# Optimization experiments

Hardware: AMD Instinct MI355X
Metric: run time of the kernel (lower is better)

The kernel has to match this reference:

```python
import jax, jax.numpy as jnp
import numpy as np

N = 2048   # nodes
E = 65536  # edges (avg degree 32)
F = 7      # node_feature_dim
S = 32     # state_dim
L = 16     # latent_dim
R = 3      # message passing rounds


def setup_inputs() -> dict:
    key = jax.random.key(0)
    ks = jax.random.split(key, 12)
    g = lambda k, shape, s: (jax.random.normal(k, shape, jnp.float32) * s)
    return dict(
        x=g(ks[0], (N, F), 1.0),
        edge_index=jax.random.randint(ks[1], (2, E), 0, N, dtype=jnp.int32),
        # input_net Linear(F->S)
        W_in=g(ks[2], (F, S), 0.3), b_in=jnp.zeros((S,), jnp.float32),
        # message nets: R x Linear(S->S)
        W_msg=g(ks[3], (R, S, S), 0.15), b_msg=jnp.zeros((R, S), jnp.float32),
        # GRU cells: R x (weight_ih, weight_hh) stored (in, 3*S) with torch gate order r,z,n
        W_ih=g(ks[4], (R, S, 3 * S), 0.15), W_hh=g(ks[5], (R, S, 3 * S), 0.15),
        b_ih=jnp.zeros((R, 3 * S), jnp.float32), b_hh=jnp.zeros((R, 3 * S), jnp.float32),
        # mu / logstd heads Linear(S->L)
        W_mu=g(ks[6], (S, L), 0.15), b_mu=jnp.zeros((L,), jnp.float32),
        W_ls=g(ks[7], (S, L), 0.15), b_ls=jnp.zeros((L,), jnp.float32),
        # decoder: Linear(2L->L), ReLU, Linear(L->1)
        W_d1=g(ks[8], (2 * L, L), 0.2), b_d1=jnp.zeros((L,), jnp.float32),
        W_d2=g(ks[9], (L, 1), 0.2), b_d2=jnp.zeros((1,), jnp.float32),
    )


def reference(x, edge_index, W_in, b_in, W_msg, b_msg, W_ih, W_hh, b_ih, b_hh,
              W_mu, b_mu, W_ls, b_ls, W_d1, b_d1, W_d2, b_d2):
    src, dst = edge_index[0], edge_index[1]
    # encoder
    state = jax.nn.relu(x @ W_in + b_in)  # [N, S]
    for r in range(R):
        message = jax.nn.relu(state @ W_msg[r] + b_msg[r])          # [N, S]
        aggregated = jax.ops.segment_sum(jnp.take(message, src, axis=0), dst,
                                         num_segments=N)            # [N, S]
        # GRUCell(aggregated, state), torch gate order: r, z, n
        gx = aggregated @ W_ih[r] + b_ih[r]                         # [N, 3S]
        gh = state @ W_hh[r] + b_hh[r]                              # [N, 3S]
        xr, xz, xn = jnp.split(gx, 3, axis=-1)
        hr, hz, hn = jnp.split(gh, 3, axis=-1)
        rg = jax.nn.sigmoid(xr + hr)
        zg = jax.nn.sigmoid(xz + hz)
        ng = jnp.tanh(xn + rg * hn)
        new_h = (1.0 - zg) * ng + zg * state
        state = state + new_h
    mu = state @ W_mu + b_mu        # [N, L]
    logstd = state @ W_ls + b_ls    # [N, L]
    # eval-mode reparameterize: z = mu
    z = mu
    # decode: Linear on concat([z_i, z_j]) == z_i @ W_d1[:L] + z_j @ W_d1[L:]
    a = z @ W_d1[:L]   # [N, L] contribution of row latent
    b = z @ W_d1[L:]   # [N, L] contribution of col latent
    h = jax.nn.relu(a[:, None, :] + b[None, :, :] + b_d1)  # [N, N, L]
    adj_logits = (h @ W_d2)[..., 0] + b_d2[0]              # [N, N]
    adj_logits = (adj_logits + adj_logits.T) / 2.0
    adj_recon = jax.nn.sigmoid(adj_logits)
    return (adj_recon, mu, logstd)
```

## Files before the change

kernel.cpp:

```cpp
#include <hip/hip_runtime.h>
#include <math.h>

#define NN 2048
#define EE 65536
#define FF 7
#define SS 32
#define LL 16
#define BKT 64
#define OCAP 4096
#define NBLK 256

struct Params {
    const float *x; const int *ei;
    const float *W_in, *b_in, *W_msg, *b_msg, *W_ih, *W_hh, *b_ih, *b_hh;
    const float *W_mu, *b_mu, *W_ls, *b_ls, *W_d1, *b_d1;
    float *msg0, *msg1, *msg2, *Abuf, *Bbuf;
    int *cnt, *ocnt, *olist, *bucket, *flags, *go;
    float *out_mu, *out_ls;
};

__device__ __forceinline__ float fsig(float x) { return 1.f / (1.f + __expf(-x)); }
__device__ __forceinline__ float ftanh(float x) { return 1.f - 2.f / (__expf(2.f * x) + 1.f); }

__device__ __forceinline__ void stwt(float* p, float v) {
    __hip_atomic_store(p, v, __ATOMIC_RELAXED, __HIP_MEMORY_SCOPE_SYSTEM);
}
__device__ __forceinline__ void stwt_i(int* p, int v) {
    __hip_atomic_store(p, v, __ATOMIC_RELAXED, __HIP_MEMORY_SCOPE_SYSTEM);
}
__device__ __forceinline__ int ldsys(const int* p) {
    return __hip_atomic_load(p, __ATOMIC_RELAXED, __HIP_MEMORY_SCOPE_SYSTEM);
}

__device__ __forceinline__ void gbar(int* flags, int* go, int phase) {
    __syncthreads();
    if (blockIdx.x == 0) {
        if (threadIdx.x < 64) {
            if (threadIdx.x == 0)
                stwt_i(flags + 0, phase);
            int l = threadIdx.x;
            for (;;) {
                int a = ldsys(flags + l);
                int b = ldsys(flags + l + 64);
                int c = ldsys(flags + l + 128);
                int d = ldsys(flags + l + 192);
                if (__all(a >= phase && b >= phase && c >= phase && d >= phase)) break;
                __builtin_amdgcn_s_sleep(2);
            }
            if (threadIdx.x == 0)
                stwt_i(go, phase);
        }
    } else if (threadIdx.x == 0) {
        stwt_i(flags + blockIdx.x, phase);
        while (ldsys(go) < phase) __builtin_amdgcn_s_sleep(8);
    }
    __syncthreads();
}

__device__ __forceinline__ float gather_gru(int s, int deg, int i0, int i1,
        const int* ocnt, const int* olist, int n,
        const float* msg_in, float h0,
        const float* Wih, const float* Whh,
        const float* bih, const float* bhh) {
    float acc = 0.f;
#pragma unroll
    for (int k = 0; k < 32; k++) {
        int bsrc = __shfl(i0, k, 32);
        int src = (k < deg) ? bsrc : 0;
        float v = msg_in[src * SS + s];
        acc += (k < deg) ? v : 0.f;
    }
#pragma unroll
    for (int k = 0; k < 32; k++) {
        int kk = 32 + k;
        int bsrc = __shfl(i1, k, 32);
        int src = (kk < deg) ? bsrc : 0;
        float v = msg_in[src * SS + s];
        acc += (kk < deg) ? v : 0.f;
    }
    if (deg > BKT) {
        int oc = *ocnt; if (oc > OCAP) oc = OCAP;
        for (int i = 0; i < oc; i++)
            if (olist[2 * i + 1] == n) acc += msg_in[olist[2 * i] * SS + s];
    }
    float xr = bih[s], xz = bih[SS + s], xn = bih[2 * SS + s];
    float hr = bhh[s], hz = bhh[SS + s], hn = bhh[2 * SS + s];
#pragma unroll
    for (int k = 0; k < SS; k++) {
        float av = __shfl(acc, k, 32);
        float hv = __shfl(h0, k, 32);
        const float* wi = Wih + k * 3 * SS;
        const float* wh = Whh + k * 3 * SS;
        xr += av * wi[s];
        xz += av * wi[SS + s];
        xn += av * wi[2 * SS + s];
        hr += hv * wh[s];
        hz += hv * wh[SS + s];
        hn += hv * wh[2 * SS + s];
    }
    float rg = fsig(xr + hr);
    float zg = fsig(xz + hz);
    float ng = ftanh(xn + rg * hn);
    return h0 + (1.f - zg) * ng + zg * h0;
}

__global__ void __launch_bounds__(256) gnn(Params p) {
    int tid = threadIdx.x;
    int gid = blockIdx.x * 256 + tid;
    int n = gid >> 5, s = gid & 31;

    float stc;

    {
        int e = gid;
        int src = p.ei[e], dst = p.ei[EE + e];
        int slot = atomicAdd(&p.cnt[dst], 1);
        if (slot < BKT) stwt_i(&p.bucket[dst * BKT + slot], src);
        else {
            int oi = atomicAdd(p.ocnt, 1);
            if (oi < OCAP) { stwt_i(&p.olist[2 * oi], src); stwt_i(&p.olist[2 * oi + 1], dst); }
        }
        const float* xr = p.x + n * FF;
        float acc = p.b_in[s];
#pragma unroll
        for (int k = 0; k < FF; k++) acc += xr[k] * p.W_in[k * SS + s];
        stc = fmaxf(acc, 0.f);
        float m = p.b_msg[s];
#pragma unroll
        for (int k = 0; k < SS; k++) m += __shfl(stc, k, 32) * p.W_msg[k * SS + s];
        stwt(&p.msg0[n * SS + s], fmaxf(m, 0.f));
    }
    gbar(p.flags, p.go, 1);

    int deg = p.cnt[n];
    int i0 = p.bucket[n * BKT + s];
    int i1 = p.bucket[n * BKT + SS + s];

    {
        stc = gather_gru(s, deg, i0, i1, p.ocnt, p.olist, n, p.msg0, stc,
                         p.W_ih, p.W_hh, p.b_ih, p.b_hh);
        const float* Wm = p.W_msg + 1 * SS * SS;
        const float* bm = p.b_msg + 1 * SS;
        float mv = bm[s];
#pragma unroll
        for (int k = 0; k < SS; k++) mv += __shfl(stc, k, 32) * Wm[k * SS + s];
        stwt(&p.msg1[n * SS + s], fmaxf(mv, 0.f));
    }
    gbar(p.flags, p.go, 2);

    {
        stc = gather_gru(s, deg, i0, i1, p.ocnt, p.olist, n, p.msg1, stc,
                         p.W_ih + SS * 3 * SS, p.W_hh + SS * 3 * SS,
                         p.b_ih + 3 * SS, p.b_hh + 3 * SS);
        const float* Wm = p.W_msg + 2 * SS * SS;
        const float* bm = p.b_msg + 2 * SS;
        float mv = bm[s];
#pragma unroll
        for (int k = 0; k < SS; k++) mv += __shfl(stc, k, 32) * Wm[k * SS + s];
        stwt(&p.msg2[n * SS + s], fmaxf(mv, 0.f));
    }
    gbar(p.flags, p.go, 3);

    {
        stc = gather_gru(s, deg, i0, i1, p.ocnt, p.olist, n, p.msg2, stc,
                         p.W_ih + 2 * SS * 3 * SS, p.W_hh + 2 * SS * 3 * SS,
                         p.b_ih + 2 * 3 * SS, p.b_hh + 2 * 3 * SS);
        int l = s & 15;
        const float* W = (s < 16) ? p.W_mu : p.W_ls;
        float v = (s < 16) ? p.b_mu[l] : p.b_ls[l];
#pragma unroll
        for (int k = 0; k < SS; k++) v += __shfl(stc, k, 32) * W[k * LL + l];
        if (s < 16) p.out_mu[n * LL + l] = v; else p.out_ls[n * LL + l] = v;
        const float* Wd = p.W_d1 + ((s < 16) ? 0 : LL * LL);
        float ab = (s < 16) ? p.b_d1[l] : 0.f;
#pragma unroll
        for (int k = 0; k < LL; k++) ab += __shfl(v, k, 32) * Wd[k * LL + l];
        if (s < 16) p.Abuf[n * LL + l] = ab; else p.Bbuf[n * LL + l] = ab;
    }
}

__global__ __launch_bounds__(256) void dec_kernel(const float* __restrict__ Abuf,
                                                  const float* __restrict__ Bbuf,
                                                  const float* __restrict__ W_d2,
                                                  const float* __restrict__ b_d2,
                                                  float* __restrict__ out) {
    __shared__ float ldsAj[LL * 64];
    __shared__ float ldsBj[LL * 64];
    __shared__ float ldsT[64 * 65];
    int t = blockIdx.x;
    int bi = (int)((65.f - sqrtf(4225.f - 8.f * (float)t)) * 0.5f);
    if (bi < 0) bi = 0;
    if (bi > 31) bi = 31;
    while (bi > 0 && (65 * bi - bi * bi) / 2 > t) bi--;
    while (bi < 31 && (65 * (bi + 1) - (bi + 1) * (bi + 1)) / 2 <= t) bi++;
    int bj = bi + (t - (65 * bi - bi * bi) / 2);
    int i0 = bi * 64, j0 = bj * 64;
    int tid = threadIdx.x;

    {
        int jr = tid >> 2, q = tid & 3;
        float4 va = ((const float4*)(Abuf + (size_t)(j0 + jr) * LL))[q];
        float4 vb = ((const float4*)(Bbuf + (size_t)(j0 + jr) * LL))[q];
        int l4 = q * 4;
        ldsAj[(l4 + 0) * 64 + jr] = va.x; ldsAj[(l4 + 1) * 64 + jr] = va.y;
        ldsAj[(l4 + 2) * 64 + jr] = va.z; ldsAj[(l4 + 3) * 64 + jr] = va.w;
        ldsBj[(l4 + 0) * 64 + jr] = vb.x; ldsBj[(l4 + 1) * 64 + jr] = vb.y;
        ldsBj[(l4 + 2) * 64 + jr] = vb.z; ldsBj[(l4 + 3) * 64 + jr] = vb.w;
    }
    __syncthreads();

    int jo = tid & 63;
    int ig = tid >> 6;
    float aj[LL], bjr[LL], w[LL];
#pragma unroll
    for (int l = 0; l < LL; l++) {
        aj[l] = ldsAj[l * 64 + jo];
        bjr[l] = ldsBj[l * 64 + jo];
        w[l] = W_d2[l];
    }
    float bd2 = b_d2[0];
    int j = j0 + jo;

#pragma unroll 2
    for (int ii = 0; ii < 16; ii++) {
        int i = i0 + ig * 16 + ii;
        const float4* Ai4 = (const float4*)(Abuf + (size_t)i * LL);
        const float4* Bi4 = (const float4*)(Bbuf + (size_t)i * LL);
        float4 a0 = Ai4[0], a1 = Ai4[1], a2 = Ai4[2], a3 = Ai4[3];
        float4 b0 = Bi4[0], b1 = Bi4[1], b2 = Bi4[2], b3 = Bi4[3];
        float ai[LL] = {a0.x, a0.y, a0.z, a0.w, a1.x, a1.y, a1.z, a1.w,
                        a2.x, a2.y, a2.z, a2.w, a3.x, a3.y, a3.z, a3.w};
        float bi_[LL] = {b0.x, b0.y, b0.z, b0.w, b1.x, b1.y, b1.z, b1.w,
                         b2.x, b2.y, b2.z, b2.w, b3.x, b3.y, b3.z, b3.w};
        float accij = 0.f, accji = 0.f;
#pragma unroll
        for (int l = 0; l < LL; l++) {
            accij += w[l] * fmaxf(ai[l] + bjr[l], 0.f);
            accji += w[l] * fmaxf(aj[l] + bi_[l], 0.f);
        }
        float logit = 0.5f * (accij + accji) + bd2;
        float p = 1.f / (1.f + __expf(-logit));
        out[(size_t)i * NN + j] = p;
        ldsT[jo * 65 + ig * 16 + ii] = p;
    }

    if (bi != bj) {
        __syncthreads();
        int jj = tid >> 2, qi = tid & 3;
        float v[16];
#pragma unroll
        for (int m = 0; m < 16; m++) v[m] = ldsT[jj * 65 + qi * 16 + m];
        float4* dst = (float4*)(out + (size_t)(j0 + jj) * NN + i0 + qi * 16);
#pragma unroll
        for (int q4 = 0; q4 < 4; q4++)
            dst[q4] = make_float4(v[4 * q4], v[4 * q4 + 1], v[4 * q4 + 2], v[4 * q4 + 3]);
    }
}

extern "C" void kernel_launch(void* const* d_in, const int* in_sizes, int n_in,
                              void* d_out, int out_size, void* d_ws, size_t ws_size,
                              hipStream_t stream) {
    Params p;
    p.x     = (const float*)d_in[0];
    p.ei    = (const int*)d_in[1];
    p.W_in  = (const float*)d_in[2];
    p.b_in  = (const float*)d_in[3];
    p.W_msg = (const float*)d_in[4];
    p.b_msg = (const float*)d_in[5];
    p.W_ih  = (const float*)d_in[6];
    p.W_hh  = (const float*)d_in[7];
    p.b_ih  = (const float*)d_in[8];
    p.b_hh  = (const float*)d_in[9];
    p.W_mu  = (const float*)d_in[10];
    p.b_mu  = (const float*)d_in[11];
    p.W_ls  = (const float*)d_in[12];
    p.b_ls  = (const float*)d_in[13];
    p.W_d1  = (const float*)d_in[14];
    p.b_d1  = (const float*)d_in[15];
    const float* W_d2 = (const float*)d_in[16];
    const float* b_d2 = (const float*)d_in[17];

    float* ws = (float*)d_ws;
    p.msg0 = ws;
    p.msg1 = p.msg0 + NN * SS;
    p.msg2 = p.msg1 + NN * SS;
    p.Abuf = p.msg2 + NN * SS;
    p.Bbuf = p.Abuf + NN * LL;
    p.cnt  = (int*)(p.Bbuf + NN * LL);
    p.ocnt = p.cnt + NN;
    p.flags = p.ocnt + 1;
    p.go   = p.flags + NBLK;
    p.olist = p.go + 4;
    p.bucket = p.olist + 2 * OCAP;

    float* out_adj = (float*)d_out;
    p.out_mu  = out_adj + (size_t)NN * NN;
    p.out_ls  = p.out_mu + NN * LL;

    hipMemsetAsync(p.cnt, 0, (NN + 1 + NBLK + 4) * sizeof(int), stream);

    gnn<<<NBLK, 256, 0, stream>>>(p);

    dec_kernel<<<528, 256, 0, stream>>>(p.Abuf, p.Bbuf, W_d2, b_d2, out_adj);
}
```

Measured before the change: 60.17 us.

## Split each node's gather across a full 64-lane wave with 512 blocks

The encoder now assigns one 64-lane wavefront per node instead of 32 lanes, doubling the block count to 512. Each half-wave gathers half of the bucketed neighbours, and the halves are combined with a cross-lane xor shuffle, which shortens the serial gather chain per thread. Atomic loads and stores used for flags and buffers move from system scope to agent scope to make them cheaper. The grid barrier now polls 512 flags, and two blocks per CU must fit co-resident for the persistent grid barrier to avoid deadlock.

New measurement: 78.28 us. 30.1% more time.

```diff
diff --git a/kernel.cpp b/kernel.cpp
--- a/kernel.cpp
+++ b/kernel.cpp
@@ -8,7 +8,7 @@
 #define LL 16
 #define BKT 64
 #define OCAP 4096
-#define NBLK 256
+#define NBLK 512
 
 struct Params {
     const float *x; const int *ei;
@@ -23,32 +23,32 @@
 __device__ __forceinline__ float ftanh(float x) { return 1.f - 2.f / (__expf(2.f * x) + 1.f); }
 
 __device__ __forceinline__ void stwt(float* p, float v) {
-    __hip_atomic_store(p, v, __ATOMIC_RELAXED, __HIP_MEMORY_SCOPE_SYSTEM);
+    __hip_atomic_store(p, v, __ATOMIC_RELAXED, __HIP_MEMORY_SCOPE_AGENT);
 }
 __device__ __forceinline__ void stwt_i(int* p, int v) {
-    __hip_atomic_store(p, v, __ATOMIC_RELAXED, __HIP_MEMORY_SCOPE_SYSTEM);
+    __hip_atomic_store(p, v, __ATOMIC_RELAXED, __HIP_MEMORY_SCOPE_AGENT);
 }
 __device__ __forceinline__ int ldsys(const int* p) {
-    return __hip_atomic_load(p, __ATOMIC_RELAXED, __HIP_MEMORY_SCOPE_SYSTEM);
+    return __hip_atomic_load(p, __ATOMIC_RELAXED, __HIP_MEMORY_SCOPE_AGENT);
 }
 
 __device__ __forceinline__ void gbar(int* flags, int* go, int phase) {
     __syncthreads();
     if (blockIdx.x == 0) {
         if (threadIdx.x < 64) {
-            if (threadIdx.x == 0)
-                stwt_i(flags + 0, phase);
+            if (threadIdx.x == 0) stwt_i(flags + 0, phase);
             int l = threadIdx.x;
             for (;;) {
-                int a = ldsys(flags + l);
-                int b = ldsys(flags + l + 64);
-                int c = ldsys(flags + l + 128);
-                int d = ldsys(flags + l + 192);
-                if (__all(a >= phase && b >= phase && c >= phase && d >= phase)) break;
+                int mn = 0x7fffffff;
+#pragma unroll
+                for (int q = 0; q < NBLK / 64; q++) {
+                    int v = ldsys(flags + l + q * 64);
+                    mn = (v < mn) ? v : mn;
+                }
+                if (__all(mn >= phase)) break;
                 __builtin_amdgcn_s_sleep(2);
             }
-            if (threadIdx.x == 0)
-                stwt_i(go, phase);
+            if (threadIdx.x == 0) stwt_i(go, phase);
         }
     } else if (threadIdx.x == 0) {
         stwt_i(flags + blockIdx.x, phase);
@@ -57,7 +57,7 @@
     __syncthreads();
 }
 
-__device__ __forceinline__ float gather_gru(int s, int deg, int i0, int i1,
+__device__ __forceinline__ float gather_gru64(int s, int hsel, int deg, int myidx,
         const int* ocnt, const int* olist, int n,
         const float* msg_in, float h0,
         const float* Wih, const float* Whh,
@@ -65,24 +65,19 @@
     float acc = 0.f;
 #pragma unroll
     for (int k = 0; k < 32; k++) {
-        int bsrc = __shfl(i0, k, 32);
-        int src = (k < deg) ? bsrc : 0;
+        int slot = hsel + k;
+        int bsrc = __shfl(myidx, slot, 64);
+        bool valid = slot < deg;
+        int src = valid ? bsrc : 0;
         float v = msg_in[src * SS + s];
-        acc += (k < deg) ? v : 0.f;
-    }
-#pragma unroll
-    for (int k = 0; k < 32; k++) {
-        int kk = 32 + k;
-        int bsrc = __shfl(i1, k, 32);
-        int src = (kk < deg) ? bsrc : 0;
-        float v = msg_in[src * SS + s];
-        acc += (kk < deg) ? v : 0.f;
-    }
-    if (deg > BKT) {
-        int oc = *ocnt; if (oc > OCAP) oc = OCAP;
+        acc += valid ? v : 0.f;
+    }
+    if (deg > BKT && hsel == 0) {
+        int oc = ldsys(ocnt); if (oc > OCAP) oc = OCAP;
         for (int i = 0; i < oc; i++)
-            if (olist[2 * i + 1] == n) acc += msg_in[olist[2 * i] * SS + s];
-    }
+            if (ldsys(&olist[2 * i + 1]) == n) acc += msg_in[ldsys(&olist[2 * i]) * SS + s];
+    }
+    acc += __shfl_xor(acc, 32, 64);
     float xr = bih[s], xz = bih[SS + s], xn = bih[2 * SS + s];
     float hr = bhh[s], hz = bhh[SS + s], hn = bhh[2 * SS + s];
 #pragma unroll
@@ -104,21 +99,25 @@
     return h0 + (1.f - zg) * ng + zg * h0;
 }
 
-__global__ void __launch_bounds__(256) gnn(Params p) {
+__global__ void __launch_bounds__(256, 2) gnn(Params p) {
     int tid = threadIdx.x;
     int gid = blockIdx.x * 256 + tid;
-    int n = gid >> 5, s = gid & 31;
+    int n = gid >> 6;
+    int lane = gid & 63;
+    int s = lane & 31;
+    int hsel = lane & 32;
 
     float stc;
 
     {
-        int e = gid;
-        int src = p.ei[e], dst = p.ei[EE + e];
-        int slot = atomicAdd(&p.cnt[dst], 1);
-        if (slot < BKT) stwt_i(&p.bucket[dst * BKT + slot], src);
-        else {
-            int oi = atomicAdd(p.ocnt, 1);
-            if (oi < OCAP) { stwt_i(&p.olist[2 * oi], src); stwt_i(&p.olist[2 * oi + 1], dst); }
+        if (gid < EE) {
+            int src = p.ei[gid], dst = p.ei[EE + gid];
+            int slot = atomicAdd(&p.cnt[dst], 1);
+            if (slot < BKT) stwt_i(&p.bucket[dst * BKT + slot], src);
+            else {
+                int oi = atomicAdd(p.ocnt, 1);
+                if (oi < OCAP) { stwt_i(&p.olist[2 * oi], src); stwt_i(&p.olist[2 * oi + 1], dst); }
+            }
         }
         const float* xr = p.x + n * FF;
         float acc = p.b_in[s];
@@ -128,54 +127,53 @@
         float m = p.b_msg[s];
 #pragma unroll
         for (int k = 0; k < SS; k++) m += __shfl(stc, k, 32) * p.W_msg[k * SS + s];
-        stwt(&p.msg0[n * SS + s], fmaxf(m, 0.f));
+        if (lane < 32) stwt(&p.msg0[n * SS + s], fmaxf(m, 0.f));
     }
     gbar(p.flags, p.go, 1);
 
     int deg = p.cnt[n];
-    int i0 = p.bucket[n * BKT + s];
-    int i1 = p.bucket[n * BKT + SS + s];
-
-    {
-        stc = gather_gru(s, deg, i0, i1, p.ocnt, p.olist, n, p.msg0, stc,
-                         p.W_ih, p.W_hh, p.b_ih, p.b_hh);
+    int myidx = ldsys(&p.bucket[n * BKT + lane]);
+
+    {
+        stc = gather_gru64(s, hsel, deg, myidx, p.ocnt, p.olist, n, p.msg0, stc,
+                           p.W_ih, p.W_hh, p.b_ih, p.b_hh);
         const float* Wm = p.W_msg + 1 * SS * SS;
         const float* bm = p.b_msg + 1 * SS;
         float mv = bm[s];
 #pragma unroll
         for (int k = 0; k < SS; k++) mv += __shfl(stc, k, 32) * Wm[k * SS + s];
-        stwt(&p.msg1[n * SS + s], fmaxf(mv, 0.f));
+        if (lane < 32) stwt(&p.msg1[n * SS + s], fmaxf(mv, 0.f));
     }
     gbar(p.flags, p.go, 2);
 
     {
-        stc = gather_gru(s, deg, i0, i1, p.ocnt, p.olist, n, p.msg1, stc,
-                         p.W_ih + SS * 3 * SS, p.W_hh + SS * 3 * SS,
-                         p.b_ih + 3 * SS, p.b_hh + 3 * SS);
+        stc = gather_gru64(s, hsel, deg, myidx, p.ocnt, p.olist, n, p.msg1, stc,
+                           p.W_ih + SS * 3 * SS, p.W_hh + SS * 3 * SS,
+                           p.b_ih + 3 * SS, p.b_hh + 3 * SS);
         const float* Wm = p.W_msg + 2 * SS * SS;
         const float* bm = p.b_msg + 2 * SS;
         float mv = bm[s];
 #pragma unroll
         for (int k = 0; k < SS; k++) mv += __shfl(stc, k, 32) * Wm[k * SS + s];
-        stwt(&p.msg2[n * SS + s], fmaxf(mv, 0.f));
+        if (lane < 32) stwt(&p.msg2[n * SS + s], fmaxf(mv, 0.f));
     }
     gbar(p.flags, p.go, 3);
 
     {
-        stc = gather_gru(s, deg, i0, i1, p.ocnt, p.olist, n, p.msg2, stc,
-                         p.W_ih + 2 * SS * 3 * SS, p.W_hh + 2 * SS * 3 * SS,
-                         p.b_ih + 2 * 3 * SS, p.b_hh + 2 * 3 * SS);
+        stc = gather_gru64(s, hsel, deg, myidx, p.ocnt, p.olist, n, p.msg2, stc,
+                           p.W_ih + 2 * SS * 3 * SS, p.W_hh + 2 * SS * 3 * SS,
+                           p.b_ih + 2 * 3 * SS, p.b_hh + 2 * 3 * SS);
         int l = s & 15;
         const float* W = (s < 16) ? p.W_mu : p.W_ls;
         float v = (s < 16) ? p.b_mu[l] : p.b_ls[l];
 #pragma unroll
         for (int k = 0; k < SS; k++) v += __shfl(stc, k, 32) * W[k * LL + l];
-        if (s < 16) p.out_mu[n * LL + l] = v; else p.out_ls[n * LL + l] = v;
+        if (lane < 32) { if (s < 16) p.out_mu[n * LL + l] = v; else p.out_ls[n * LL + l] = v; }
         const float* Wd = p.W_d1 + ((s < 16) ? 0 : LL * LL);
         float ab = (s < 16) ? p.b_d1[l] : 0.f;
 #pragma unroll
         for (int k = 0; k < LL; k++) ab += __shfl(v, k, 32) * Wd[k * LL + l];
-        if (s < 16) p.Abuf[n * LL + l] = ab; else p.Bbuf[n * LL + l] = ab;
+        if (lane < 32) { if (s < 16) p.Abuf[n * LL + l] = ab; else p.Bbuf[n * LL + l] = ab; }
     }
 }
 
```

## Replace grid barriers between GRU rounds with per-node readiness flags

Applied to the files above, without the earlier changes.

Removes the second and third grid-wide barriers. Each node publishes a sequence flag once its message vector is written, and consumers poll the flags of only their neighbours before gathering. Atomic memory scope is also narrowed from system to agent, which should make the stores, loads and barrier polls cheaper. The cost is many more flag polls per warp, plus a risk of ordering bugs, because only a relaxed store after a vmcnt wait is used to publish the messages.

Measured after the change: 82.50 us. 37.1% more time.

```diff
diff --git a/kernel.cpp b/kernel.cpp
--- a/kernel.cpp
+++ b/kernel.cpp
@@ -15,7 +15,7 @@
     const float *W_in, *b_in, *W_msg, *b_msg, *W_ih, *W_hh, *b_ih, *b_hh;
     const float *W_mu, *b_mu, *W_ls, *b_ls, *W_d1, *b_d1;
     float *msg0, *msg1, *msg2, *Abuf, *Bbuf;
-    int *cnt, *ocnt, *olist, *bucket, *flags, *go;
+    int *cnt, *ocnt, *olist, *bucket, *flags, *go, *seq;
     float *out_mu, *out_ls;
 };
 
@@ -23,21 +23,20 @@
 __device__ __forceinline__ float ftanh(float x) { return 1.f - 2.f / (__expf(2.f * x) + 1.f); }
 
 __device__ __forceinline__ void stwt(float* p, float v) {
-    __hip_atomic_store(p, v, __ATOMIC_RELAXED, __HIP_MEMORY_SCOPE_SYSTEM);
+    __hip_atomic_store(p, v, __ATOMIC_RELAXED, __HIP_MEMORY_SCOPE_AGENT);
 }
 __device__ __forceinline__ void stwt_i(int* p, int v) {
-    __hip_atomic_store(p, v, __ATOMIC_RELAXED, __HIP_MEMORY_SCOPE_SYSTEM);
+    __hip_atomic_store(p, v, __ATOMIC_RELAXED, __HIP_MEMORY_SCOPE_AGENT);
 }
 __device__ __forceinline__ int ldsys(const int* p) {
-    return __hip_atomic_load(p, __ATOMIC_RELAXED, __HIP_MEMORY_SCOPE_SYSTEM);
+    return __hip_atomic_load(p, __ATOMIC_RELAXED, __HIP_MEMORY_SCOPE_AGENT);
 }
 
 __device__ __forceinline__ void gbar(int* flags, int* go, int phase) {
     __syncthreads();
     if (blockIdx.x == 0) {
         if (threadIdx.x < 64) {
-            if (threadIdx.x == 0)
-                stwt_i(flags + 0, phase);
+            if (threadIdx.x == 0) stwt_i(flags + 0, phase);
             int l = threadIdx.x;
             for (;;) {
                 int a = ldsys(flags + l);
@@ -47,8 +46,7 @@
                 if (__all(a >= phase && b >= phase && c >= phase && d >= phase)) break;
                 __builtin_amdgcn_s_sleep(2);
             }
-            if (threadIdx.x == 0)
-                stwt_i(go, phase);
+            if (threadIdx.x == 0) stwt_i(go, phase);
         }
     } else if (threadIdx.x == 0) {
         stwt_i(flags + blockIdx.x, phase);
@@ -57,8 +55,23 @@
     __syncthreads();
 }
 
+__device__ __forceinline__ void wait_ready(const int* seq, int i0, int i1,
+                                           int deg, int s, int r) {
+    bool need0 = s < deg;
+    bool need1 = (SS + s) < deg;
+    int j0 = need0 ? i0 : 0;
+    int j1 = need1 ? i1 : 0;
+    for (;;) {
+        bool ok0 = !need0 || (ldsys(&seq[j0]) >= r);
+        bool ok1 = !need1 || (ldsys(&seq[j1]) >= r);
+        if (__all(ok0 && ok1)) break;
+        __builtin_amdgcn_s_sleep(1);
+    }
+    asm volatile("" ::: "memory");
+}
+
 __device__ __forceinline__ float gather_gru(int s, int deg, int i0, int i1,
-        const int* ocnt, const int* olist, int n,
+        const int* ocnt, const int* olist, const int* seq, int pollRnd, int n,
         const float* msg_in, float h0,
         const float* Wih, const float* Whh,
         const float* bih, const float* bhh) {
@@ -79,9 +92,14 @@
         acc += (kk < deg) ? v : 0.f;
     }
     if (deg > BKT) {
-        int oc = *ocnt; if (oc > OCAP) oc = OCAP;
+        int oc = ldsys(ocnt); if (oc > OCAP) oc = OCAP;
         for (int i = 0; i < oc; i++)
-            if (olist[2 * i + 1] == n) acc += msg_in[olist[2 * i] * SS + s];
+            if (ldsys(&olist[2 * i + 1]) == n) {
+                int src = ldsys(&olist[2 * i]);
+                if (pollRnd > 0)
+                    while (ldsys(&seq[src]) < pollRnd) __builtin_amdgcn_s_sleep(1);
+                acc += msg_in[src * SS + s];
+            }
     }
     float xr = bih[s], xz = bih[SS + s], xn = bih[2 * SS + s];
     float hr = bhh[s], hz = bhh[SS + s], hn = bhh[2 * SS + s];
@@ -112,8 +130,7 @@
     float stc;
 
     {
-        int e = gid;
-        int src = p.ei[e], dst = p.ei[EE + e];
+        int src = p.ei[gid], dst = p.ei[EE + gid];
         int slot = atomicAdd(&p.cnt[dst], 1);
         if (slot < BKT) stwt_i(&p.bucket[dst * BKT + slot], src);
         else {
@@ -133,11 +150,11 @@
     gbar(p.flags, p.go, 1);
 
     int deg = p.cnt[n];
-    int i0 = p.bucket[n * BKT + s];
-    int i1 = p.bucket[n * BKT + SS + s];
-
-    {
-        stc = gather_gru(s, deg, i0, i1, p.ocnt, p.olist, n, p.msg0, stc,
+    int i0 = ldsys(&p.bucket[n * BKT + s]);
+    int i1 = ldsys(&p.bucket[n * BKT + SS + s]);
+
+    {
+        stc = gather_gru(s, deg, i0, i1, p.ocnt, p.olist, p.seq, 0, n, p.msg0, stc,
                          p.W_ih, p.W_hh, p.b_ih, p.b_hh);
         const float* Wm = p.W_msg + 1 * SS * SS;
         const float* bm = p.b_msg + 1 * SS;
@@ -145,11 +162,13 @@
 #pragma unroll
         for (int k = 0; k < SS; k++) mv += __shfl(stc, k, 32) * Wm[k * SS + s];
         stwt(&p.msg1[n * SS + s], fmaxf(mv, 0.f));
-    }
-    gbar(p.flags, p.go, 2);
-
-    {
-        stc = gather_gru(s, deg, i0, i1, p.ocnt, p.olist, n, p.msg1, stc,
+        asm volatile("s_waitcnt vmcnt(0)" ::: "memory");
+        if (s == 0) stwt_i(&p.seq[n], 1);
+    }
+
+    {
+        wait_ready(p.seq, i0, i1, deg, s, 1);
+        stc = gather_gru(s, deg, i0, i1, p.ocnt, p.olist, p.seq, 1, n, p.msg1, stc,
                          p.W_ih + SS * 3 * SS, p.W_hh + SS * 3 * SS,
                          p.b_ih + 3 * SS, p.b_hh + 3 * SS);
         const float* Wm = p.W_msg + 2 * SS * SS;
@@ -158,11 +177,13 @@
 #pragma unroll
         for (int k = 0; k < SS; k++) mv += __shfl(stc, k, 32) * Wm[k * SS + s];
         stwt(&p.msg2[n * SS + s], fmaxf(mv, 0.f));
-    }
-    gbar(p.flags, p.go, 3);
-
-    {
-        stc = gather_gru(s, deg, i0, i1, p.ocnt, p.olist, n, p.msg2, stc,
+        asm volatile("s_waitcnt vmcnt(0)" ::: "memory");
+        if (s == 0) stwt_i(&p.seq[n], 2);
+    }
+
+    {
+        wait_ready(p.seq, i0, i1, deg, s, 2);
+        stc = gather_gru(s, deg, i0, i1, p.ocnt, p.olist, p.seq, 2, n, p.msg2, stc,
                          p.W_ih + 2 * SS * 3 * SS, p.W_hh + 2 * SS * 3 * SS,
                          p.b_ih + 2 * 3 * SS, p.b_hh + 2 * 3 * SS);
         int l = s & 15;
@@ -290,14 +311,15 @@
     p.ocnt = p.cnt + NN;
     p.flags = p.ocnt + 1;
     p.go   = p.flags + NBLK;
-    p.olist = p.go + 4;
+    p.seq  = p.go + 4;
+    p.olist = p.seq + NN;
     p.bucket = p.olist + 2 * OCAP;
 
     float* out_adj = (float*)d_out;
     p.out_mu  = out_adj + (size_t)NN * NN;
     p.out_ls  = p.out_mu + NN * LL;
 
-    hipMemsetAsync(p.cnt, 0, (NN + 1 + NBLK + 4) * sizeof(int), stream);
+    hipMemsetAsync(p.cnt, 0, (NN + 1 + NBLK + 4 + NN) * sizeof(int), stream);
 
     gnn<<<NBLK, 256, 0, stream>>>(p);
 
```
